# Kernel optimization log

Measured on AMD Instinct MI355X. Metric: run time of the kernel, lower is better.

Reference implementation:

```python
import jax, jax.numpy as jnp
import numpy as np


def setup_inputs() -> dict:
    key = jax.random.key(0)
    k1, k2, k3, k4 = jax.random.split(key, 4)
    B, M, S, Q = 128, 200, 20, 20
    H, V, D = 3, 50000, 128  # max_hops, num_vocab, embedding_dim
    story = jax.random.randint(k1, (B, M, S), 0, V)
    query = jax.random.randint(k2, (B, Q), 0, V)
    # (max_hops+1) embedding tables, init normal(0, 0.1) as in torch code
    E = jax.random.normal(k3, (H + 1, V, D), dtype=jnp.float32) * 0.1
    # (max_hops+1) temporal encodings [max_story_size, D], normal(0, 0.1)
    T = jax.random.normal(k4, (H + 1, M, D), dtype=jnp.float32) * 0.1
    return {"story": story, "query": query, "E": E, "T": T}


def reference(story, query, E, T):
    max_hops = E.shape[0] - 1
    # u1 = sum over query tokens of B-embedding (hop-0 table)
    u = jnp.sum(E[0][query], axis=1)  # [B, D]
    for hop in range(max_hops):
        # memory: A-embed story, sum over words, add temporal encoding
        m = jnp.sum(E[hop][story], axis=2) + T[hop]        # [B, M, D]
        # attention over memories (legacy F.softmax on 2D -> dim=1)
        uTm = jnp.einsum('bmd,bd->bm', m, u)               # [B, M]
        proba = jax.nn.softmax(uTm, axis=1)
        # output memory representation
        c = jnp.sum(E[hop + 1][story], axis=2) + T[hop + 1]  # [B, M, D]
        o = jnp.einsum('bm,bmd->bd', proba, c)             # [B, D]
        u = u + o
    ahat = u @ E[-1].T  # [B, V]
    return ahat, jax.nn.softmax(ahat, axis=1)
```

## Files before the change

### kernel.cpp

```cpp
#include <hip/hip_runtime.h>
#include <float.h>


constexpr int Bn = 128;
constexpr int Mn = 200;
constexpr int Sn = 20;
constexpr int Qn = 20;
constexpr int Hn = 3;
constexpr int Vn = 50000;
constexpr int Dn = 128;
constexpr int CH = 100;

constexpr int GTILE = 128;
constexpr int NT    = (Vn + GTILE - 1) / GTILE;
constexpr int SMCHK = 10;

constexpr size_t MSUM_ELEMS = (size_t)(Hn + 1) * Bn * Mn * Dn;
constexpr size_t SMWS_ELEMS = (size_t)NT * Bn * 2;

__global__ __launch_bounds__(256)
void msum_kernel(const int* __restrict__ story, const float* __restrict__ E,
                 const float* __restrict__ T, float* __restrict__ msum) {
    int slot = threadIdx.x >> 5;
    int l    = threadIdx.x & 31;
    int row  = blockIdx.x * 8 + slot;
    int t    = row / (Bn * Mn);
    int rem  = row - t * (Bn * Mn);
    int b    = rem / Mn;
    int m    = rem - b * Mn;

    const int* st = story + (b * Mn + m) * Sn;
    const float4* Tv = (const float4*)(T) + (size_t)(t * Mn + m) * 32;
    const float4* Et = (const float4*)(E) + (size_t)t * Vn * 32;

    float4 acc = Tv[l];
    #pragma unroll
    for (int s = 0; s < Sn; ++s) {
        float4 e = Et[(size_t)st[s] * 32 + l];
        acc.x += e.x; acc.y += e.y; acc.z += e.z; acc.w += e.w;
    }
    ((float4*)msum)[(size_t)row * 32 + l] = acc;
}

__global__ __launch_bounds__(1024)
void hops_kernel(const int* __restrict__ query, const float* __restrict__ E,
                 const float* __restrict__ msum, float* __restrict__ ufin) {
    __shared__ __align__(16) float u[Dn];
    __shared__ float sc[Mn];
    __shared__ float op[8 * Dn];
    __shared__ float red[16];
    __shared__ float bc[2];

    const int b    = blockIdx.x;
    const int tid  = threadIdx.x;
    const int wave = tid >> 6;
    const int lane = tid & 63;
    const int d    = tid & (Dn - 1);
    const int g    = tid >> 7;

    if (tid < Dn) {
        float acc = 0.f;
        const int* q = query + b * Qn;
        #pragma unroll
        for (int j = 0; j < Qn; ++j)
            acc += E[(size_t)q[j] * Dn + tid];
        u[tid] = acc;
    }
    __syncthreads();

    for (int hop = 0; hop < Hn; ++hop) {
        const float* mrow = msum + ((size_t)hop * Bn + b) * (size_t)(Mn * Dn);
        float2 u2 = *(const float2*)(u + 2 * lane);

        for (int q = wave; q < Mn / 4; q += 16) {
            const float* r = mrow + (size_t)q * 4 * Dn;
            float2 a0 = *(const float2*)(r + 0 * Dn + 2 * lane);
            float2 a1 = *(const float2*)(r + 1 * Dn + 2 * lane);
            float2 a2 = *(const float2*)(r + 2 * Dn + 2 * lane);
            float2 a3 = *(const float2*)(r + 3 * Dn + 2 * lane);
            float p0 = a0.x * u2.x + a0.y * u2.y;
            float p1 = a1.x * u2.x + a1.y * u2.y;
            float p2 = a2.x * u2.x + a2.y * u2.y;
            float p3 = a3.x * u2.x + a3.y * u2.y;
            #pragma unroll
            for (int off = 32; off; off >>= 1) {
                p0 += __shfl_down(p0, off, 64);
                p1 += __shfl_down(p1, off, 64);
                p2 += __shfl_down(p2, off, 64);
                p3 += __shfl_down(p3, off, 64);
            }
            if (lane == 0) {
                sc[4 * q + 0] = p0; sc[4 * q + 1] = p1;
                sc[4 * q + 2] = p2; sc[4 * q + 3] = p3;
            }
        }
        __syncthreads();

        float v = (tid < Mn) ? sc[tid] : -FLT_MAX;
        float mx = v;
        #pragma unroll
        for (int off = 32; off; off >>= 1) mx = fmaxf(mx, __shfl_down(mx, off, 64));
        if (lane == 0) red[wave] = mx;
        __syncthreads();
        if (tid == 0) {
            float m0 = red[0];
            #pragma unroll
            for (int i = 1; i < 16; ++i) m0 = fmaxf(m0, red[i]);
            bc[0] = m0;
        }
        __syncthreads();
        float rmax = bc[0];
        float e = (tid < Mn) ? __expf(v - rmax) : 0.f;
        float sm = e;
        #pragma unroll
        for (int off = 32; off; off >>= 1) sm += __shfl_down(sm, off, 64);
        if (lane == 0) red[wave] = sm;
        __syncthreads();
        if (tid == 0) {
            float s = 0.f;
            #pragma unroll
            for (int i = 0; i < 16; ++i) s += red[i];
            bc[1] = s;
        }
        __syncthreads();
        float inv = 1.f / bc[1];
        if (tid < Mn) sc[tid] = e * inv;
        __syncthreads();

        const float* crow = msum + ((size_t)(hop + 1) * Bn + b) * (size_t)(Mn * Dn);
        float acc = 0.f;
        for (int m = g; m < Mn; m += 8)
            acc += sc[m] * crow[m * Dn + d];
        op[g * Dn + d] = acc;
        __syncthreads();
        if (tid < Dn) {
            float s = 0.f;
            #pragma unroll
            for (int i = 0; i < 8; ++i) s += op[i * Dn + tid];
            u[tid] += s;
        }
        __syncthreads();
    }
    if (tid < Dn) ufin[b * Dn + tid] = u[tid];
}

__global__ __launch_bounds__(1024)
void hops_fused_kernel(const int* __restrict__ story, const int* __restrict__ query,
                       const float* __restrict__ E, const float* __restrict__ T,
                       float* __restrict__ ufin) {
    __shared__ __align__(16) float tile[CH * Dn];
    __shared__ float u[Dn];
    __shared__ float sc[Mn];
    __shared__ float op[8 * Dn];
    __shared__ float red[16];
    __shared__ float bc[2];

    const int b    = blockIdx.x;
    const int tid  = threadIdx.x;
    const int wave = tid >> 6;
    const int lane = tid & 63;
    const int d    = tid & (Dn - 1);
    const int g    = tid >> 7;
    const int slot = tid >> 5;
    const int l    = tid & 31;
    const int* st  = story + b * (Mn * Sn);

    if (tid < Dn) {
        float acc = 0.f;
        const int* q = query + b * Qn;
        #pragma unroll
        for (int j = 0; j < Qn; ++j)
            acc += E[(size_t)q[j] * Dn + tid];
        u[tid] = acc;
    }

    auto build = [&](int t, int base) {
        const float4* Et = (const float4*)(E) + (size_t)t * Vn * 32;
        const float4* Tt = (const float4*)(T) + (size_t)t * Mn * 32;
        for (int m = base + slot; m < base + CH; m += 32) {
            const int* sm = st + m * Sn;
            float4 acc = Tt[(size_t)m * 32 + l];
            #pragma unroll
            for (int s = 0; s < Sn; ++s) {
                float4 e = Et[(size_t)sm[s] * 32 + l];
                acc.x += e.x; acc.y += e.y; acc.z += e.z; acc.w += e.w;
            }
            ((float4*)tile)[(m - base) * 32 + l] = acc;
        }
    };
    auto scores = [&](int base) {
        for (int m = base + wave; m < base + CH; m += 16) {
            float p = tile[(m - base) * Dn + lane]      * u[lane]
                    + tile[(m - base) * Dn + lane + 64] * u[lane + 64];
            #pragma unroll
            for (int off = 32; off; off >>= 1) p += __shfl_down(p, off, 64);
            if (lane == 0) sc[m] = p;
        }
    };

    for (int hop = 0; hop < Hn; ++hop) {
        if (hop == 0) {
            build(0, 0);  __syncthreads(); scores(0);  __syncthreads();
            build(0, CH); __syncthreads(); scores(CH); __syncthreads();
        } else {
            scores(CH); __syncthreads();
            build(hop, 0); __syncthreads(); scores(0); __syncthreads();
        }

        float v = (tid < Mn) ? sc[tid] : -FLT_MAX;
        float mx = v;
        #pragma unroll
        for (int off = 32; off; off >>= 1) mx = fmaxf(mx, __shfl_down(mx, off, 64));
        if (lane == 0) red[wave] = mx;
        __syncthreads();
        if (tid == 0) {
            float m0 = red[0];
            #pragma unroll
            for (int i = 1; i < 16; ++i) m0 = fmaxf(m0, red[i]);
            bc[0] = m0;
        }
        __syncthreads();
        float rmax = bc[0];
        float e = (tid < Mn) ? __expf(v - rmax) : 0.f;
        float sm = e;
        #pragma unroll
        for (int off = 32; off; off >>= 1) sm += __shfl_down(sm, off, 64);
        if (lane == 0) red[wave] = sm;
        __syncthreads();
        if (tid == 0) {
            float s = 0.f;
            #pragma unroll
            for (int i = 0; i < 16; ++i) s += red[i];
            bc[1] = s;
        }
        __syncthreads();
        float inv = 1.f / bc[1];
        if (tid < Mn) sc[tid] = e * inv;

        float oacc = 0.f;
        build(hop + 1, 0);
        __syncthreads();
        for (int m = g; m < CH; m += 8)
            oacc += sc[m] * tile[m * Dn + d];
        __syncthreads();
        build(hop + 1, CH);
        __syncthreads();
        for (int m = CH + g; m < 2 * CH; m += 8)
            oacc += sc[m] * tile[(m - CH) * Dn + d];
        op[g * Dn + d] = oacc;
        __syncthreads();
        if (tid < Dn) {
            float s = 0.f;
            #pragma unroll
            for (int i = 0; i < 8; ++i) s += op[i * Dn + tid];
            u[tid] += s;
        }
        __syncthreads();
    }

    if (tid < Dn) ufin[b * Dn + tid] = u[tid];
}

constexpr int KC   = 32;
constexpr int LSTR = 140;
__device__ __forceinline__ int ldsCol(int c) { return c + 4 * (c >> 5); }

__global__ __launch_bounds__(256)
void ahat_gemm_kernel(const float* __restrict__ E, const float* __restrict__ ufin,
                      float* __restrict__ out, float* __restrict__ ws2) {
    __shared__ __align__(16) float uA[KC * LSTR];
    __shared__ __align__(16) float eB[KC * LSTR];
    const float* E3 = E + (size_t)Hn * Vn * Dn;

    const int tid   = threadIdx.x;
    const int tr    = tid & 15;
    const int tc    = tid >> 4;
    const int vbase = blockIdx.x * GTILE;

    const int f4 = tid & 7;
    const int rr = tid >> 3;

    float acc[8][8];
    #pragma unroll
    for (int i = 0; i < 8; ++i)
        #pragma unroll
        for (int j = 0; j < 8; ++j) acc[i][j] = 0.f;

    for (int kb = 0; kb < Dn; kb += KC) {
        #pragma unroll
        for (int i = 0; i < 4; ++i) {
            int r   = rr + 32 * i;
            int col = ldsCol(r);
            float4 uv = *(const float4*)(ufin + (size_t)r * Dn + kb + f4 * 4);
            uA[(f4 * 4 + 0) * LSTR + col] = uv.x;
            uA[(f4 * 4 + 1) * LSTR + col] = uv.y;
            uA[(f4 * 4 + 2) * LSTR + col] = uv.z;
            uA[(f4 * 4 + 3) * LSTR + col] = uv.w;
        }
        #pragma unroll
        for (int i = 0; i < 4; ++i) {
            int r  = rr + 32 * i;
            int vg = vbase + r; if (vg > Vn - 1) vg = Vn - 1;
            int col = ldsCol(r);
            float4 ev = *(const float4*)(E3 + (size_t)vg * Dn + kb + f4 * 4);
            eB[(f4 * 4 + 0) * LSTR + col] = ev.x;
            eB[(f4 * 4 + 1) * LSTR + col] = ev.y;
            eB[(f4 * 4 + 2) * LSTR + col] = ev.z;
            eB[(f4 * 4 + 3) * LSTR + col] = ev.w;
        }
        __syncthreads();
        const int ca = ldsCol(tr * 8);
        const int cb = ldsCol(tc * 8);
        #pragma unroll 2
        for (int k = 0; k < KC; ++k) {
            float4 a0 = *(const float4*)&uA[k * LSTR + ca];
            float4 a1 = *(const float4*)&uA[k * LSTR + ca + 4];
            float4 b0 = *(const float4*)&eB[k * LSTR + cb];
            float4 b1 = *(const float4*)&eB[k * LSTR + cb + 4];
            float av[8] = {a0.x, a0.y, a0.z, a0.w, a1.x, a1.y, a1.z, a1.w};
            float bv[8] = {b0.x, b0.y, b0.z, b0.w, b1.x, b1.y, b1.z, b1.w};
            #pragma unroll
            for (int i = 0; i < 8; ++i)
                #pragma unroll
                for (int j = 0; j < 8; ++j)
                    acc[i][j] += av[i] * bv[j];
        }
        __syncthreads();
    }

    const int  v0    = vbase + tc * 8;
    const bool valid = v0 < Vn;
    if (valid) {
        #pragma unroll
        for (int i = 0; i < 8; ++i) {
            int bb = tr * 8 + i;
            *(float4*)(out + (size_t)bb * Vn + v0) =
                make_float4(acc[i][0], acc[i][1], acc[i][2], acc[i][3]);
            *(float4*)(out + (size_t)bb * Vn + v0 + 4) =
                make_float4(acc[i][4], acc[i][5], acc[i][6], acc[i][7]);
        }
    }

    if (ws2) {
        #pragma unroll
        for (int i = 0; i < 8; ++i) {
            float tm = -FLT_MAX, ts = 0.f;
            if (valid) {
                #pragma unroll
                for (int j = 0; j < 8; ++j) tm = fmaxf(tm, acc[i][j]);
                #pragma unroll
                for (int j = 0; j < 8; ++j) ts += __expf(acc[i][j] - tm);
            }
            uA[tc * 128 + tr * 8 + i] = tm;
            eB[tc * 128 + tr * 8 + i] = ts;
        }
        __syncthreads();
        if (tid < Bn) {
            float M = -FLT_MAX;
            #pragma unroll
            for (int t = 0; t < 16; ++t) M = fmaxf(M, uA[t * 128 + tid]);
            float S = 0.f;
            #pragma unroll
            for (int t = 0; t < 16; ++t)
                S += eB[t * 128 + tid] * __expf(uA[t * 128 + tid] - M);
            float2* w = (float2*)ws2;
            w[(size_t)blockIdx.x * Bn + tid] = make_float2(M, S);
        }
    }
}

__global__ __launch_bounds__(256)
void softmax_merge_kernel(const float* __restrict__ ahat, const float* __restrict__ ws2,
                          float* __restrict__ osm) {
    __shared__ float redm[4], reds[4];
    __shared__ float bcM, bcI;

    const int ck   = blockIdx.x;
    const int b    = blockIdx.y;
    const int tid  = threadIdx.x;
    const int wave = tid >> 6;
    const int lane = tid & 63;

    float m = -FLT_MAX, s = 0.f;
    const float2* w = (const float2*)ws2;
    for (int i = tid; i < NT; i += 256) {
        float2 p = w[(size_t)i * Bn + b];
        float nm = fmaxf(m, p.x);
        s = s * __expf(m - nm) + p.y * __expf(p.x - nm);
        m = nm;
    }
    #pragma unroll
    for (int off = 32; off; off >>= 1) {
        float mo = __shfl_down(m, off, 64);
        float so = __shfl_down(s, off, 64);
        float nm = fmaxf(m, mo);
        s = s * __expf(m - nm) + so * __expf(mo - nm);
        m = nm;
    }
    if (lane == 0) { redm[wave] = m; reds[wave] = s; }
    __syncthreads();
    if (tid == 0) {
        float M = redm[0];
        #pragma unroll
        for (int i = 1; i < 4; ++i) M = fmaxf(M, redm[i]);
        float S = 0.f;
        #pragma unroll
        for (int i = 0; i < 4; ++i) S += reds[i] * __expf(redm[i] - M);
        bcM = M; bcI = 1.f / S;
    }
    __syncthreads();
    const float M   = bcM;
    const float inv = bcI;

    constexpr int C4 = Vn / SMCHK / 4;
    const float4* row  = (const float4*)(ahat + (size_t)b * Vn) + (size_t)ck * C4;
    float4*       orow = (float4*)(osm + (size_t)b * Vn) + (size_t)ck * C4;
    for (int v = tid; v < C4; v += 256) {
        float4 x = row[v];
        orow[v] = make_float4(__expf(x.x - M) * inv, __expf(x.y - M) * inv,
                              __expf(x.z - M) * inv, __expf(x.w - M) * inv);
    }
}

__global__ __launch_bounds__(1024)
void softmax_kernel(const float* __restrict__ ahat, float* __restrict__ osm) {
    __shared__ float redm[16];
    __shared__ float reds[16];
    __shared__ float bc2[2];

    int b    = blockIdx.x;
    int tid  = threadIdx.x;
    int wave = tid >> 6;
    int lane = tid & 63;

    const float4* row  = (const float4*)(ahat + (size_t)b * Vn);
    float4*       orow = (float4*)(osm + (size_t)b * Vn);
    constexpr int N4 = Vn / 4;

    float m = -FLT_MAX, s = 0.f;
    for (int v = tid; v < N4; v += 1024) {
        float4 x = row[v];
        float cm = fmaxf(fmaxf(x.x, x.y), fmaxf(x.z, x.w));
        if (cm > m) { s *= __expf(m - cm); m = cm; }
        s += __expf(x.x - m) + __expf(x.y - m) + __expf(x.z - m) + __expf(x.w - m);
    }
    #pragma unroll
    for (int off = 32; off; off >>= 1) {
        float mo = __shfl_down(m, off, 64);
        float so = __shfl_down(s, off, 64);
        float nm = fmaxf(m, mo);
        s = s * __expf(m - nm) + so * __expf(mo - nm);
        m = nm;
    }
    if (lane == 0) { redm[wave] = m; reds[wave] = s; }
    __syncthreads();
    if (tid == 0) {
        float M = redm[0];
        #pragma unroll
        for (int i = 1; i < 16; ++i) M = fmaxf(M, redm[i]);
        float S = 0.f;
        #pragma unroll
        for (int i = 0; i < 16; ++i) S += reds[i] * __expf(redm[i] - M);
        bc2[0] = M; bc2[1] = 1.f / S;
    }
    __syncthreads();
    float rmax = bc2[0];
    float inv  = bc2[1];

    for (int v = tid; v < N4; v += 1024) {
        float4 x = row[v];
        orow[v] = make_float4(__expf(x.x - rmax) * inv, __expf(x.y - rmax) * inv,
                              __expf(x.z - rmax) * inv, __expf(x.w - rmax) * inv);
    }
}

extern "C" void kernel_launch(void* const* d_in, const int* in_sizes, int n_in,
                              void* d_out, int out_size, void* d_ws, size_t ws_size,
                              hipStream_t stream) {
    const int*   story = (const int*)d_in[0];
    const int*   query = (const int*)d_in[1];
    const float* E     = (const float*)d_in[2];
    const float* T     = (const float*)d_in[3];

    float* out  = (float*)d_out;
    float* ufin = out + (size_t)Bn * Vn;

    const bool haveMsum = ws_size >= MSUM_ELEMS * sizeof(float);
    const bool haveSm   = ws_size >= (MSUM_ELEMS + SMWS_ELEMS) * sizeof(float);
    float* msum = (float*)d_ws;
    float* ws2  = haveSm ? ((float*)d_ws + MSUM_ELEMS) : nullptr;

    if (haveMsum) {
        msum_kernel<<<(Hn + 1) * Bn * Mn / 8, 256, 0, stream>>>(story, E, T, msum);
        hops_kernel<<<Bn, 1024, 0, stream>>>(query, E, msum, ufin);
    } else {
        hops_fused_kernel<<<Bn, 1024, 0, stream>>>(story, query, E, T, ufin);
    }

    ahat_gemm_kernel<<<NT, 256, 0, stream>>>(E, ufin, out, ws2);

    if (ws2) {
        softmax_merge_kernel<<<dim3(SMCHK, Bn), 256, 0, stream>>>(
            out, ws2, out + (size_t)Bn * Vn);
    } else {
        softmax_kernel<<<Bn, 1024, 0, stream>>>(out, out + (size_t)Bn * Vn);
    }
}
```

Measured before the change: 341.3 us.

## Stage memory tables in shared memory and reuse across hops

The hops kernel now copies each per-batch memory table into a padded LDS tile. It computes the attention scores and the weighted output sum from that tile rather than from global memory. The same staged table serves as the output memory for one hop and the input memory for the next, so each table is read from global once instead of twice. This costs about 104 KB of LDS per block and adds an extra staging pass with register buffering.

```diff
diff --git a/kernel.cpp b/kernel.cpp
--- a/kernel.cpp
+++ b/kernel.cpp
@@ -14,6 +14,8 @@
 constexpr int GTILE = 128;
 constexpr int NT    = (Vn + GTILE - 1) / GTILE;
 constexpr int SMCHK = 10;
+
+constexpr int TSTR = 130;
 
 constexpr size_t MSUM_ELEMS = (size_t)(Hn + 1) * Bn * Mn * Dn;
 constexpr size_t SMWS_ELEMS = (size_t)NT * Bn * 2;
@@ -45,9 +47,10 @@
 __global__ __launch_bounds__(1024)
 void hops_kernel(const int* __restrict__ query, const float* __restrict__ E,
                  const float* __restrict__ msum, float* __restrict__ ufin) {
-    __shared__ __align__(16) float u[Dn];
+    __shared__ __align__(16) float tileA[Mn * TSTR];
+    __shared__ float u[Dn];
     __shared__ float sc[Mn];
-    __shared__ float op[8 * Dn];
+    __shared__ float op[1024];
     __shared__ float red[16];
     __shared__ float bc[2];
 
@@ -57,6 +60,25 @@
     const int lane = tid & 63;
     const int d    = tid & (Dn - 1);
     const int g    = tid >> 7;
+    const int dq   = tid >> 8;
+    const int mm   = tid & 255;
+
+    auto stage = [&](int t) {
+        const float* src = msum + ((size_t)t * Bn + b) * (size_t)(Mn * Dn);
+        float2 vbuf[13];
+        #pragma unroll
+        for (int k = 0; k < 13; ++k) {
+            int r = wave + 16 * k;
+            if (r < Mn)
+                vbuf[k] = *(const float2*)(src + (size_t)r * Dn + 2 * lane);
+        }
+        #pragma unroll
+        for (int k = 0; k < 13; ++k) {
+            int r = wave + 16 * k;
+            if (r < Mn)
+                *(float2*)(tileA + r * TSTR + 2 * lane) = vbuf[k];
+        }
+    };
 
     if (tid < Dn) {
         float acc = 0.f;
@@ -66,37 +88,22 @@
             acc += E[(size_t)q[j] * Dn + tid];
         u[tid] = acc;
     }
+    stage(0);
     __syncthreads();
 
     for (int hop = 0; hop < Hn; ++hop) {
-        const float* mrow = msum + ((size_t)hop * Bn + b) * (size_t)(Mn * Dn);
-        float2 u2 = *(const float2*)(u + 2 * lane);
-
-        for (int q = wave; q < Mn / 4; q += 16) {
-            const float* r = mrow + (size_t)q * 4 * Dn;
-            float2 a0 = *(const float2*)(r + 0 * Dn + 2 * lane);
-            float2 a1 = *(const float2*)(r + 1 * Dn + 2 * lane);
-            float2 a2 = *(const float2*)(r + 2 * Dn + 2 * lane);
-            float2 a3 = *(const float2*)(r + 3 * Dn + 2 * lane);
-            float p0 = a0.x * u2.x + a0.y * u2.y;
-            float p1 = a1.x * u2.x + a1.y * u2.y;
-            float p2 = a2.x * u2.x + a2.y * u2.y;
-            float p3 = a3.x * u2.x + a3.y * u2.y;
-            #pragma unroll
-            for (int off = 32; off; off >>= 1) {
-                p0 += __shfl_down(p0, off, 64);
-                p1 += __shfl_down(p1, off, 64);
-                p2 += __shfl_down(p2, off, 64);
-                p3 += __shfl_down(p3, off, 64);
-            }
-            if (lane == 0) {
-                sc[4 * q + 0] = p0; sc[4 * q + 1] = p1;
-                sc[4 * q + 2] = p2; sc[4 * q + 3] = p3;
-            }
-        }
-        __syncthreads();
-
-        float v = (tid < Mn) ? sc[tid] : -FLT_MAX;
+        if (mm < Mn) {
+            float p = 0.f;
+            #pragma unroll
+            for (int i = 0; i < 32; ++i)
+                p += tileA[mm * TSTR + dq * 32 + i] * u[dq * 32 + i];
+            op[dq * Mn + mm] = p;
+        }
+        __syncthreads();
+
+        float v = -FLT_MAX;
+        if (tid < Mn)
+            v = op[tid] + op[Mn + tid] + op[2 * Mn + tid] + op[3 * Mn + tid];
         float mx = v;
         #pragma unroll
         for (int off = 32; off; off >>= 1) mx = fmaxf(mx, __shfl_down(mx, off, 64));
@@ -125,12 +132,16 @@
         __syncthreads();
         float inv = 1.f / bc[1];
         if (tid < Mn) sc[tid] = e * inv;
-        __syncthreads();
-
-        const float* crow = msum + ((size_t)(hop + 1) * Bn + b) * (size_t)(Mn * Dn);
+
+        stage(hop + 1);
+        __syncthreads();
+
         float acc = 0.f;
-        for (int m = g; m < Mn; m += 8)
-            acc += sc[m] * crow[m * Dn + d];
+        #pragma unroll
+        for (int k = 0; k < 25; ++k) {
+            int m = g + 8 * k;
+            acc += sc[m] * tileA[m * TSTR + d];
+        }
         op[g * Dn + d] = acc;
         __syncthreads();
         if (tid < Dn) {
```

New measurement: 323.1 us. 1.06x faster.
